# Performance work log

Measured on AMD Instinct MI355X. Metric: run time of the kernel, lower is better.

The kernel has to match this reference:

```python
import jax, jax.numpy as jnp
import numpy as np

B, C, H, W = 4, 32, 32, 1024
PATCH = 21           # patch_size in spatial_correlation_sample
DIL = 2              # dilation_patch
PAD = DIL * (PATCH - 1) // 2  # 20: max displacement, zero-padded out-of-range samples


def setup_inputs() -> dict:
    key = jax.random.key(0)
    k1, k2 = jax.random.split(key)
    x1 = jax.random.normal(k1, (B, C, H, W), dtype=jnp.float32)
    x2 = jax.random.normal(k2, (B, C, H, W), dtype=jnp.float32)
    return {"x1": x1, "x2": x2}


def _correlate(x1, x2):
    # spatial_correlation_sample(kernel_size=1, patch_size=21, stride=1,
    #                            padding=0, dilation_patch=2)
    # out[b, pi, pj, h, w] = sum_c x1[b,c,h,w] * x2[b,c,h+2*(pi-10), w+2*(pj-10)]
    # with out-of-bounds x2 samples treated as zero.
    b, c, h, w = x1.shape
    x2p = jnp.pad(x2, ((0, 0), (0, 0), (PAD, PAD), (PAD, PAD)))
    chans = []
    for i in range(PATCH):      # fixed 21x21 displacement grid (static slices)
        for j in range(PATCH):
            win = jax.lax.slice(x2p, (0, 0, DIL * i, DIL * j),
                                (b, c, DIL * i + h, DIL * j + w))
            chans.append(jnp.einsum('bchw,bchw->bhw', x1, win))
    corr = jnp.stack(chans, axis=1) / c  # (b, 441, h, w), normalized by n_channels
    return jax.nn.leaky_relu(corr, negative_slope=0.1)


def reference(x1, x2):
    # CorrelationNetwork.forward returns only out_correlation; the conv/deconv
    # flow pyramid does not contribute to the returned tensor (and the
    # visualize_flow calls reference undefined symbols in the original).
    return _correlate(x1, x2)
```

## Files before the change

### kernel.cpp

```cpp
#include <hip/hip_runtime.h>
#include <stdint.h>

#define BB     4
#define CC     32
#define HH     32
#define WW     1024
#define PATCH  21
#define DIL    2
#define RAD    10
#define PADW   20
#define CHUNKC 2
#define NP     (CC / CHUNKC)
#define NGR    266
#define ROWF   (NGR * 4)
#define BUFF   (CHUNKC * ROWF)

typedef __attribute__((address_space(3))) uint32_t lds_u32_t;
typedef __attribute__((address_space(1))) const uint32_t glb_u32_t;

__device__ __forceinline__ int swz(int s) { return s ^ ((s >> 3) & 1); }

__device__ __forceinline__ void stage_dma(const float* __restrict__ x2c0,
                                          float* __restrict__ sbuf, int tid) {
#pragma unroll
    for (int t = 0; t < 3; t++) {
        const int idx = tid + t * 256;
        if (idx < CHUNKC * NGR) {
            const int c  = (idx >= NGR) ? 1 : 0;
            const int q  = idx - c * NGR;
            const int gq = swz(q);
            const int base_gran = (tid & ~63) + t * 256;
            lds_u32_t* ldst = (lds_u32_t*)(sbuf + base_gran * 4);
            const float* src = x2c0 + (size_t)c * (HH * WW) + (gq * 4 - PADW);
            if (gq >= 5 && gq <= 260)
                __builtin_amdgcn_global_load_lds((glb_u32_t*)src, ldst, 16, 0, 0);
        }
    }
}

template <int PJ0, int NT, int NACC>
__device__ __forceinline__ void compute_half(const float* __restrict__ x1p,
                                             const float* __restrict__ sbuf,
                                             int tw, float (&acc)[NACC][8]) {
    constexpr int PJ0A = PJ0 & ~1;
    constexpr int DD   = 2 * (PJ0 - PJ0A);
    constexpr int NV4  = (DD + 8 + 2 * (NT - 1) + 3) / 4;
    const int g0 = 2 * tw + PJ0A / 2;
    int ps[NV4];
#pragma unroll
    for (int r = 0; r < NV4; r++) ps[r] = 4 * swz(g0 + r);

#pragma unroll
    for (int c = 0; c < CHUNKC; c++) {
        const float* xp = x1p + (size_t)c * (HH * WW);
        float4 a0 = *(const float4*)xp;
        float4 a1 = *(const float4*)(xp + 4);
        const float a[8] = {a0.x, a0.y, a0.z, a0.w, a1.x, a1.y, a1.z, a1.w};
        const float* row = sbuf + c * ROWF;
        float win[NV4 * 4];
#pragma unroll
        for (int r = 0; r < NV4; r++)
            *(float4*)&win[4 * r] = *(const float4*)(row + ps[r]);
#pragma unroll
        for (int j = 0; j < NT; j++)
#pragma unroll
            for (int k = 0; k < 8; k++)
                acc[j][k] = fmaf(a[k], win[DD + k + 2 * j], acc[j][k]);
    }
}

template <int NT, int NACC>
__device__ __forceinline__ void epilogue(float* __restrict__ outp,
                                         const float (&acc)[NACC][8], float inv_c) {
#pragma unroll
    for (int j = 0; j < NT; j++) {
        float4 o0, o1;
        float* p0 = (float*)&o0;
        float* p1 = (float*)&o1;
#pragma unroll
        for (int k = 0; k < 4; k++) {
            float v0 = acc[j][k] * inv_c;
            float v1 = acc[j][4 + k] * inv_c;
            p0[k] = v0 > 0.f ? v0 : 0.1f * v0;
            p1[k] = v1 > 0.f ? v1 : 0.1f * v1;
        }
        *(float4*)(outp + (size_t)j * HH * WW)     = o0;
        *(float4*)(outp + (size_t)j * HH * WW + 4) = o1;
    }
}

template <int PJ0_LO, int NT_LO, int PJ0_HI, int NT_HI>
__device__ __forceinline__ void corr_body(const float* __restrict__ x1,
                                          const float* __restrict__ x2,
                                          float* __restrict__ out,
                                          float* __restrict__ sx2) {
    const int tid = threadIdx.x;
    const int tw  = tid & 127;
    const int th2 = tid >> 7;
    const int h   = blockIdx.x;
    const int bp  = blockIdx.y;
    const int b   = bp / PATCH;
    const int pi  = bp - b * PATCH;
    const int r2  = h + DIL * (pi - RAD);
    const int w8  = tw * 8;
    const int PJ0 = th2 ? PJ0_HI : PJ0_LO;
    const int NT  = th2 ? NT_HI : NT_LO;

    float* outp = out + (((size_t)(b * PATCH * PATCH + pi * PATCH + PJ0)) * HH + h) * WW + w8;

    if ((unsigned)r2 >= (unsigned)HH) {
        float4 z = make_float4(0.f, 0.f, 0.f, 0.f);
        for (int j = 0; j < NT; j++) {
            *(float4*)(outp + (size_t)j * HH * WW)     = z;
            *(float4*)(outp + (size_t)j * HH * WW + 4) = z;
        }
        return;
    }

    if (tid < 40) {
        const int rr = tid / 10, g = tid % 10;
        const int slot = (g < 5) ? g : (256 + g);
        float4 z = make_float4(0.f, 0.f, 0.f, 0.f);
        *(float4*)(sx2 + rr * ROWF + 4 * slot) = z;
    }

    const float* x2base = x2 + ((size_t)(b * CC) * HH + r2) * WW;
    const float* x1base = x1 + ((size_t)(b * CC) * HH + h) * WW + w8;

    stage_dma(x2base, sx2, tid);
    __syncthreads();

    float acc[NT_LO][8];
#pragma unroll
    for (int j = 0; j < NT_LO; j++)
#pragma unroll
        for (int k = 0; k < 8; k++) acc[j][k] = 0.f;

    for (int p = 0; p < NP; p++) {
        if (p + 1 < NP)
            stage_dma(x2base + (size_t)(p + 1) * CHUNKC * HH * WW,
                      sx2 + ((p + 1) & 1) * BUFF, tid);
        const float* bufc = sx2 + (p & 1) * BUFF;
        const float* x1p  = x1base + (size_t)p * CHUNKC * HH * WW;
        if (th2 == 0) compute_half<PJ0_LO, NT_LO>(x1p, bufc, tw, acc);
        else          compute_half<PJ0_HI, NT_HI>(x1p, bufc, tw, acc);
        if (p + 1 < NP) __syncthreads();
    }

    const float inv_c = 1.0f / (float)CC;
    if (th2 == 0) epilogue<NT_LO>(outp, acc, inv_c);
    else          epilogue<NT_HI>(outp, acc, inv_c);
}

__global__ __launch_bounds__(256, 6)
void corr_kernel(const float* __restrict__ x1, const float* __restrict__ x2,
                 float* __restrict__ out) {
    __shared__ float sx2[2 * BUFF];
    if (blockIdx.z == 0)      corr_body<0, 4, 4, 4>(x1, x2, out, sx2);
    else if (blockIdx.z == 1) corr_body<8, 4, 12, 4>(x1, x2, out, sx2);
    else                      corr_body<16, 3, 19, 2>(x1, x2, out, sx2);
}

extern "C" void kernel_launch(void* const* d_in, const int* in_sizes, int n_in,
                              void* d_out, int out_size, void* d_ws, size_t ws_size,
                              hipStream_t stream) {
    const float* x1 = (const float*)d_in[0];
    const float* x2 = (const float*)d_in[1];
    float* out = (float*)d_out;

    dim3 grid(HH, BB * PATCH, 3);
    dim3 block(256, 1, 1);
    corr_kernel<<<grid, block, 0, stream>>>(x1, x2, out);
}
```

Baseline: 341.5 us.

## Merge pj split into one 512-thread block covering all 21 offsets

Replaces the three-way blockIdx.z split of pj offsets with a single 512-thread block. Four thread groups cover pj ranges 0-5, 6-10, 11-15 and 16-20, so each staged x2 row is loaded once per (b,h,pi) instead of three times. Channel chunks double to 4 per pipeline stage and the LDS swizzle gains extra bits to spread bank conflicts. This cuts redundant x2 staging and x1 reloads at the cost of more registers per thread (6x8 accumulators), fewer resident waves, and a grid remap that orders blocks by h and pi.

```diff
diff --git a/kernel.cpp b/kernel.cpp
--- a/kernel.cpp
+++ b/kernel.cpp
@@ -9,7 +9,7 @@
 #define DIL    2
 #define RAD    10
 #define PADW   20
-#define CHUNKC 2
+#define CHUNKC 4
 #define NP     (CC / CHUNKC)
 #define NGR    266
 #define ROWF   (NGR * 4)
@@ -18,18 +18,20 @@
 typedef __attribute__((address_space(3))) uint32_t lds_u32_t;
 typedef __attribute__((address_space(1))) const uint32_t glb_u32_t;
 
-__device__ __forceinline__ int swz(int s) { return s ^ ((s >> 3) & 1); }
+__device__ __forceinline__ int swz(int s) {
+    return s ^ ((s >> 3) & 1) ^ (((s >> 4) & 3) << 1);
+}
 
 __device__ __forceinline__ void stage_dma(const float* __restrict__ x2c0,
                                           float* __restrict__ sbuf, int tid) {
 #pragma unroll
     for (int t = 0; t < 3; t++) {
-        const int idx = tid + t * 256;
+        const int idx = tid + t * 512;
         if (idx < CHUNKC * NGR) {
-            const int c  = (idx >= NGR) ? 1 : 0;
+            const int c  = idx / NGR;
             const int q  = idx - c * NGR;
             const int gq = swz(q);
-            const int base_gran = (tid & ~63) + t * 256;
+            const int base_gran = (tid & ~63) + t * 512;
             lds_u32_t* ldst = (lds_u32_t*)(sbuf + base_gran * 4);
             const float* src = x2c0 + (size_t)c * (HH * WW) + (gq * 4 - PADW);
             if (gq >= 5 && gq <= 260)
@@ -38,25 +40,22 @@
     }
 }
 
-template <int PJ0, int NT, int NACC>
-__device__ __forceinline__ void compute_half(const float* __restrict__ x1p,
-                                             const float* __restrict__ sbuf,
-                                             int tw, float (&acc)[NACC][8]) {
+template <int PJ0, int NT>
+__device__ __forceinline__ void compute_pass(const float* __restrict__ x1p,
+                                             const float* __restrict__ bufc,
+                                             const int (&ps)[5],
+                                             float (&acc)[6][8]) {
     constexpr int PJ0A = PJ0 & ~1;
     constexpr int DD   = 2 * (PJ0 - PJ0A);
     constexpr int NV4  = (DD + 8 + 2 * (NT - 1) + 3) / 4;
-    const int g0 = 2 * tw + PJ0A / 2;
-    int ps[NV4];
-#pragma unroll
-    for (int r = 0; r < NV4; r++) ps[r] = 4 * swz(g0 + r);
-
+    static_assert(NV4 <= 5, "ps[] too small");
 #pragma unroll
     for (int c = 0; c < CHUNKC; c++) {
         const float* xp = x1p + (size_t)c * (HH * WW);
         float4 a0 = *(const float4*)xp;
         float4 a1 = *(const float4*)(xp + 4);
         const float a[8] = {a0.x, a0.y, a0.z, a0.w, a1.x, a1.y, a1.z, a1.w};
-        const float* row = sbuf + c * ROWF;
+        const float* row = bufc + c * ROWF;
         float win[NV4 * 4];
 #pragma unroll
         for (int r = 0; r < NV4; r++)
@@ -69,9 +68,9 @@
     }
 }
 
-template <int NT, int NACC>
+template <int NT>
 __device__ __forceinline__ void epilogue(float* __restrict__ outp,
-                                         const float (&acc)[NACC][8], float inv_c) {
+                                         const float (&acc)[6][8], float inv_c) {
 #pragma unroll
     for (int j = 0; j < NT; j++) {
         float4 o0, o1;
@@ -89,40 +88,49 @@
     }
 }
 
-template <int PJ0_LO, int NT_LO, int PJ0_HI, int NT_HI>
-__device__ __forceinline__ void corr_body(const float* __restrict__ x1,
-                                          const float* __restrict__ x2,
-                                          float* __restrict__ out,
-                                          float* __restrict__ sx2) {
+__global__ __launch_bounds__(512, 4)
+void corr_kernel(const float* __restrict__ x1, const float* __restrict__ x2,
+                 float* __restrict__ out) {
+    __shared__ float sx2[2 * BUFF];
+
     const int tid = threadIdx.x;
     const int tw  = tid & 127;
-    const int th2 = tid >> 7;
-    const int h   = blockIdx.x;
-    const int bp  = blockIdx.y;
-    const int b   = bp / PATCH;
-    const int pi  = bp - b * PATCH;
+    const int th4 = tid >> 7;
+
+    const int b   = blockIdx.x >> 1;
+    const int hh  = blockIdx.x & 1;
+    const int by  = blockIdx.y;
+    const int pi  = by % PATCH;
+    const int h   = hh * 16 + by / PATCH;
     const int r2  = h + DIL * (pi - RAD);
     const int w8  = tw * 8;
-    const int PJ0 = th2 ? PJ0_HI : PJ0_LO;
-    const int NT  = th2 ? NT_HI : NT_LO;
 
-    float* outp = out + (((size_t)(b * PATCH * PATCH + pi * PATCH + PJ0)) * HH + h) * WW + w8;
+    const int PJ0r = (th4 == 0) ? 0 : (th4 == 1) ? 6 : (th4 == 2) ? 11 : 16;
+    const int NTr  = (th4 == 0) ? 6 : 5;
+
+    float* outp = out + (((size_t)(b * PATCH * PATCH + pi * PATCH + PJ0r)) * HH + h) * WW + w8;
 
     if ((unsigned)r2 >= (unsigned)HH) {
         float4 z = make_float4(0.f, 0.f, 0.f, 0.f);
-        for (int j = 0; j < NT; j++) {
+        for (int j = 0; j < NTr; j++) {
             *(float4*)(outp + (size_t)j * HH * WW)     = z;
             *(float4*)(outp + (size_t)j * HH * WW + 4) = z;
         }
         return;
     }
 
-    if (tid < 40) {
+    if (tid < 80) {
         const int rr = tid / 10, g = tid % 10;
         const int slot = (g < 5) ? g : (256 + g);
         float4 z = make_float4(0.f, 0.f, 0.f, 0.f);
         *(float4*)(sx2 + rr * ROWF + 4 * slot) = z;
     }
+
+    const int pj0a2 = (th4 == 0) ? 0 : (th4 == 1) ? 3 : (th4 == 2) ? 5 : 8;
+    const int g0 = 2 * tw + pj0a2;
+    int ps[5];
+#pragma unroll
+    for (int r = 0; r < 5; r++) ps[r] = 4 * swz(g0 + r);
 
     const float* x2base = x2 + ((size_t)(b * CC) * HH + r2) * WW;
     const float* x1base = x1 + ((size_t)(b * CC) * HH + h) * WW + w8;
@@ -130,9 +138,9 @@
     stage_dma(x2base, sx2, tid);
     __syncthreads();
 
-    float acc[NT_LO][8];
+    float acc[6][8];
 #pragma unroll
-    for (int j = 0; j < NT_LO; j++)
+    for (int j = 0; j < 6; j++)
 #pragma unroll
         for (int k = 0; k < 8; k++) acc[j][k] = 0.f;
 
@@ -142,23 +150,18 @@
                       sx2 + ((p + 1) & 1) * BUFF, tid);
         const float* bufc = sx2 + (p & 1) * BUFF;
         const float* x1p  = x1base + (size_t)p * CHUNKC * HH * WW;
-        if (th2 == 0) compute_half<PJ0_LO, NT_LO>(x1p, bufc, tw, acc);
-        else          compute_half<PJ0_HI, NT_HI>(x1p, bufc, tw, acc);
+        if (th4 == 0)      compute_pass<0,  6>(x1p, bufc, ps, acc);
+        else if (th4 == 1) compute_pass<6,  5>(x1p, bufc, ps, acc);
+        else if (th4 == 2) compute_pass<11, 5>(x1p, bufc, ps, acc);
+        else               compute_pass<16, 5>(x1p, bufc, ps, acc);
         if (p + 1 < NP) __syncthreads();
     }
 
     const float inv_c = 1.0f / (float)CC;
-    if (th2 == 0) epilogue<NT_LO>(outp, acc, inv_c);
-    else          epilogue<NT_HI>(outp, acc, inv_c);
-}
-
-__global__ __launch_bounds__(256, 6)
-void corr_kernel(const float* __restrict__ x1, const float* __restrict__ x2,
-                 float* __restrict__ out) {
-    __shared__ float sx2[2 * BUFF];
-    if (blockIdx.z == 0)      corr_body<0, 4, 4, 4>(x1, x2, out, sx2);
-    else if (blockIdx.z == 1) corr_body<8, 4, 12, 4>(x1, x2, out, sx2);
-    else                      corr_body<16, 3, 19, 2>(x1, x2, out, sx2);
+    if (th4 == 0)      epilogue<6>(outp, acc, inv_c);
+    else if (th4 == 1) epilogue<5>(outp, acc, inv_c);
+    else if (th4 == 2) epilogue<5>(outp, acc, inv_c);
+    else               epilogue<5>(outp, acc, inv_c);
 }
 
 extern "C" void kernel_launch(void* const* d_in, const int* in_sizes, int n_in,
@@ -168,7 +171,7 @@
     const float* x2 = (const float*)d_in[1];
     float* out = (float*)d_out;
 
-    dim3 grid(HH, BB * PATCH, 3);
-    dim3 block(256, 1, 1);
+    dim3 grid(8, (PATCH * 16), 1);
+    dim3 block(512, 1, 1);
     corr_kernel<<<grid, block, 0, stream>>>(x1, x2, out);
 }
```

After: 650.5 us. 90.5% more time.

## Index blocks by x2 row and share staged row across two output rows

Applied to the files above, without the earlier changes.

Blocks are now indexed by the x2 source row r2 instead of the output row h. Each staged x2 row in LDS then serves two (pi, h) output pairs that read the same row, halving the x2 staging per output. Each thread computes a 2x2 tile of pj displacements for two rows, and the grid becomes 72x32x6, with many blocks exiting early or idling on out-of-range slots. This cuts LDS and DMA traffic per output, at the cost of more accumulators, lower occupancy (launch bounds drop from 6 to 5) and wasted blocks.

```diff
diff --git a/kernel.cpp b/kernel.cpp
--- a/kernel.cpp
+++ b/kernel.cpp
@@ -6,7 +6,6 @@
 #define HH     32
 #define WW     1024
 #define PATCH  21
-#define DIL    2
 #define RAD    10
 #define PADW   20
 #define CHUNKC 2
@@ -14,13 +13,14 @@
 #define NGR    266
 #define ROWF   (NGR * 4)
 #define BUFF   (CHUNKC * ROWF)
+#define CSTR   (HH * WW)
 
 typedef __attribute__((address_space(3))) uint32_t lds_u32_t;
 typedef __attribute__((address_space(1))) const uint32_t glb_u32_t;
 
 __device__ __forceinline__ int swz(int s) { return s ^ ((s >> 3) & 1); }
 
-__device__ __forceinline__ void stage_dma(const float* __restrict__ x2c0,
+__device__ __forceinline__ void stage_dma(const float* __restrict__ src0,
                                           float* __restrict__ sbuf, int tid) {
 #pragma unroll
     for (int t = 0; t < 3; t++) {
@@ -30,89 +30,62 @@
             const int q  = idx - c * NGR;
             const int gq = swz(q);
             const int base_gran = (tid & ~63) + t * 256;
-            lds_u32_t* ldst = (lds_u32_t*)(sbuf + base_gran * 4);
-            const float* src = x2c0 + (size_t)c * (HH * WW) + (gq * 4 - PADW);
+            lds_u32_t* dst = (lds_u32_t*)(sbuf + base_gran * 4);
+            const float* src = src0 + (size_t)c * CSTR + (gq * 4 - PADW);
             if (gq >= 5 && gq <= 260)
-                __builtin_amdgcn_global_load_lds((glb_u32_t*)src, ldst, 16, 0, 0);
+                __builtin_amdgcn_global_load_lds((glb_u32_t*)src, dst, 16, 0, 0);
         }
     }
 }
 
-template <int PJ0, int NT, int NACC>
-__device__ __forceinline__ void compute_half(const float* __restrict__ x1p,
-                                             const float* __restrict__ sbuf,
-                                             int tw, float (&acc)[NACC][8]) {
-    constexpr int PJ0A = PJ0 & ~1;
-    constexpr int DD   = 2 * (PJ0 - PJ0A);
-    constexpr int NV4  = (DD + 8 + 2 * (NT - 1) + 3) / 4;
-    const int g0 = 2 * tw + PJ0A / 2;
-    int ps[NV4];
-#pragma unroll
-    for (int r = 0; r < NV4; r++) ps[r] = 4 * swz(g0 + r);
+__global__ __launch_bounds__(256, 5)
+void corr_kernel(const float* __restrict__ x1, const float* __restrict__ x2,
+                 float* __restrict__ out) {
+    __shared__ float sx2[2 * BUFF + 16];
 
-#pragma unroll
-    for (int c = 0; c < CHUNKC; c++) {
-        const float* xp = x1p + (size_t)c * (HH * WW);
-        float4 a0 = *(const float4*)xp;
-        float4 a1 = *(const float4*)(xp + 4);
-        const float a[8] = {a0.x, a0.y, a0.z, a0.w, a1.x, a1.y, a1.z, a1.w};
-        const float* row = sbuf + c * ROWF;
-        float win[NV4 * 4];
-#pragma unroll
-        for (int r = 0; r < NV4; r++)
-            *(float4*)&win[4 * r] = *(const float4*)(row + ps[r]);
-#pragma unroll
-        for (int j = 0; j < NT; j++)
-#pragma unroll
-            for (int k = 0; k < 8; k++)
-                acc[j][k] = fmaf(a[k], win[DD + k + 2 * j], acc[j][k]);
-    }
-}
-
-template <int NT, int NACC>
-__device__ __forceinline__ void epilogue(float* __restrict__ outp,
-                                         const float (&acc)[NACC][8], float inv_c) {
-#pragma unroll
-    for (int j = 0; j < NT; j++) {
-        float4 o0, o1;
-        float* p0 = (float*)&o0;
-        float* p1 = (float*)&o1;
-#pragma unroll
-        for (int k = 0; k < 4; k++) {
-            float v0 = acc[j][k] * inv_c;
-            float v1 = acc[j][4 + k] * inv_c;
-            p0[k] = v0 > 0.f ? v0 : 0.1f * v0;
-            p1[k] = v1 > 0.f ? v1 : 0.1f * v1;
-        }
-        *(float4*)(outp + (size_t)j * HH * WW)     = o0;
-        *(float4*)(outp + (size_t)j * HH * WW + 4) = o1;
-    }
-}
-
-template <int PJ0_LO, int NT_LO, int PJ0_HI, int NT_HI>
-__device__ __forceinline__ void corr_body(const float* __restrict__ x1,
-                                          const float* __restrict__ x2,
-                                          float* __restrict__ out,
-                                          float* __restrict__ sx2) {
     const int tid = threadIdx.x;
     const int tw  = tid & 127;
     const int th2 = tid >> 7;
-    const int h   = blockIdx.x;
-    const int bp  = blockIdx.y;
-    const int b   = bp / PATCH;
-    const int pi  = bp - b * PATCH;
-    const int r2  = h + DIL * (pi - RAD);
-    const int w8  = tw * 8;
-    const int PJ0 = th2 ? PJ0_HI : PJ0_LO;
-    const int NT  = th2 ? NT_HI : NT_LO;
+    const int r2  = (int)blockIdx.x - PADW;
+    const int b   = blockIdx.y >> 3;
+    const int s   = blockIdx.y & 7;
+    const int z   = blockIdx.z;
 
-    float* outp = out + (((size_t)(b * PATCH * PATCH + pi * PATCH + PJ0)) * HH + h) * WW + w8;
+    const int pi_hi = min(20, (r2 + 20) >> 1);
+    const int pi_lo = max(0, (r2 - 10) >> 1);
+    const int L     = pi_hi - pi_lo + 1;
+    const int e0    = 2 * s;
+    if (e0 >= L) return;
+
+    const int  pi0  = pi_hi - e0;
+    const int  h0   = r2 + 20 - 2 * pi0;
+    const bool has1 = (e0 + 1) < L;
+    const int  pi1  = pi0 - 1;
+    const int  h1   = h0 + 2;
+
+    const int  pjb    = 4 * z + 2 * th2;
+    const bool st0    = (pjb     <= 20);
+    const bool st1    = (pjb + 1 <= 20);
+    const bool active = st0;
+    const int  w8     = tw * 8;
+
+    float* out0 = out + (((size_t)(b * PATCH * PATCH + pi0 * PATCH + pjb)) * HH + h0) * WW + w8;
+    float* out1 = out + (((size_t)(b * PATCH * PATCH + pi1 * PATCH + pjb)) * HH + h1) * WW + w8;
 
     if ((unsigned)r2 >= (unsigned)HH) {
-        float4 z = make_float4(0.f, 0.f, 0.f, 0.f);
-        for (int j = 0; j < NT; j++) {
-            *(float4*)(outp + (size_t)j * HH * WW)     = z;
-            *(float4*)(outp + (size_t)j * HH * WW + 4) = z;
+        float4 zv = make_float4(0.f, 0.f, 0.f, 0.f);
+        if (active) {
+#pragma unroll
+            for (int j = 0; j < 2; j++) {
+                if (j == 0 ? st0 : st1) {
+                    *(float4*)(out0 + (size_t)j * CSTR)     = zv;
+                    *(float4*)(out0 + (size_t)j * CSTR + 4) = zv;
+                    if (has1) {
+                        *(float4*)(out1 + (size_t)j * CSTR)     = zv;
+                        *(float4*)(out1 + (size_t)j * CSTR + 4) = zv;
+                    }
+                }
+            }
         }
         return;
     }
@@ -120,45 +93,87 @@
     if (tid < 40) {
         const int rr = tid / 10, g = tid % 10;
         const int slot = (g < 5) ? g : (256 + g);
-        float4 z = make_float4(0.f, 0.f, 0.f, 0.f);
-        *(float4*)(sx2 + rr * ROWF + 4 * slot) = z;
+        *(float4*)(sx2 + rr * ROWF + 4 * slot) = make_float4(0.f, 0.f, 0.f, 0.f);
     }
 
+    const int g0 = active ? (2 * tw + 2 * z + th2) : (2 * tw);
+    int ps0 = 4 * swz(g0), ps1 = 4 * swz(g0 + 1), ps2 = 4 * swz(g0 + 2);
+
     const float* x2base = x2 + ((size_t)(b * CC) * HH + r2) * WW;
-    const float* x1base = x1 + ((size_t)(b * CC) * HH + h) * WW + w8;
+    const float* x1p0   = x1 + ((size_t)(b * CC) * HH + h0) * WW + w8;
+    const float* x1p1   = has1 ? (x1p0 + 2 * WW) : x1p0;
 
     stage_dma(x2base, sx2, tid);
     __syncthreads();
 
-    float acc[NT_LO][8];
+    float acc0[2][8], acc1[2][8];
 #pragma unroll
-    for (int j = 0; j < NT_LO; j++)
+    for (int j = 0; j < 2; j++)
 #pragma unroll
-        for (int k = 0; k < 8; k++) acc[j][k] = 0.f;
+        for (int k = 0; k < 8; k++) { acc0[j][k] = 0.f; acc1[j][k] = 0.f; }
 
     for (int p = 0; p < NP; p++) {
         if (p + 1 < NP)
-            stage_dma(x2base + (size_t)(p + 1) * CHUNKC * HH * WW,
+            stage_dma(x2base + (size_t)(p + 1) * CHUNKC * CSTR,
                       sx2 + ((p + 1) & 1) * BUFF, tid);
-        const float* bufc = sx2 + (p & 1) * BUFF;
-        const float* x1p  = x1base + (size_t)p * CHUNKC * HH * WW;
-        if (th2 == 0) compute_half<PJ0_LO, NT_LO>(x1p, bufc, tw, acc);
-        else          compute_half<PJ0_HI, NT_HI>(x1p, bufc, tw, acc);
+        if (active) {
+            const float* buf = sx2 + (p & 1) * BUFF;
+#pragma unroll
+            for (int c = 0; c < CHUNKC; c++) {
+                const float* row = buf + c * ROWF;
+                float win[12];
+                *(float4*)&win[0] = *(const float4*)(row + ps0);
+                *(float4*)&win[4] = *(const float4*)(row + ps1);
+                *(float4*)&win[8] = *(const float4*)(row + ps2);
+
+                const float* xa = x1p0 + (size_t)(CHUNKC * p + c) * CSTR;
+                const float* xb = x1p1 + (size_t)(CHUNKC * p + c) * CSTR;
+                float4 a00 = *(const float4*)xa, a01 = *(const float4*)(xa + 4);
+                float4 a10 = *(const float4*)xb, a11 = *(const float4*)(xb + 4);
+                const float a0[8] = {a00.x, a00.y, a00.z, a00.w, a01.x, a01.y, a01.z, a01.w};
+                const float a1[8] = {a10.x, a10.y, a10.z, a10.w, a11.x, a11.y, a11.z, a11.w};
+
+#pragma unroll
+                for (int j = 0; j < 2; j++)
+#pragma unroll
+                    for (int k = 0; k < 8; k++) {
+                        const float wv = win[k + 2 * j];
+                        acc0[j][k] = fmaf(a0[k], wv, acc0[j][k]);
+                        acc1[j][k] = fmaf(a1[k], wv, acc1[j][k]);
+                    }
+            }
+        }
         if (p + 1 < NP) __syncthreads();
     }
 
+    if (!active) return;
+
     const float inv_c = 1.0f / (float)CC;
-    if (th2 == 0) epilogue<NT_LO>(outp, acc, inv_c);
-    else          epilogue<NT_HI>(outp, acc, inv_c);
-}
-
-__global__ __launch_bounds__(256, 6)
-void corr_kernel(const float* __restrict__ x1, const float* __restrict__ x2,
-                 float* __restrict__ out) {
-    __shared__ float sx2[2 * BUFF];
-    if (blockIdx.z == 0)      corr_body<0, 4, 4, 4>(x1, x2, out, sx2);
-    else if (blockIdx.z == 1) corr_body<8, 4, 12, 4>(x1, x2, out, sx2);
-    else                      corr_body<16, 3, 19, 2>(x1, x2, out, sx2);
+#pragma unroll
+    for (int j = 0; j < 2; j++) {
+        if (j == 0 ? st0 : st1) {
+            float4 o0, o1, q0, q1;
+            float* po0 = (float*)&o0; float* po1 = (float*)&o1;
+            float* pq0 = (float*)&q0; float* pq1 = (float*)&q1;
+#pragma unroll
+            for (int k = 0; k < 4; k++) {
+                float v0 = acc0[j][k]     * inv_c;
+                float v1 = acc0[j][4 + k] * inv_c;
+                float u0 = acc1[j][k]     * inv_c;
+                float u1 = acc1[j][4 + k] * inv_c;
+                po0[k] = v0 > 0.f ? v0 : 0.1f * v0;
+                po1[k] = v1 > 0.f ? v1 : 0.1f * v1;
+                pq0[k] = u0 > 0.f ? u0 : 0.1f * u0;
+                pq1[k] = u1 > 0.f ? u1 : 0.1f * u1;
+            }
+            *(float4*)(out0 + (size_t)j * CSTR)     = o0;
+            *(float4*)(out0 + (size_t)j * CSTR + 4) = o1;
+            if (has1) {
+                *(float4*)(out1 + (size_t)j * CSTR)     = q0;
+                *(float4*)(out1 + (size_t)j * CSTR + 4) = q1;
+            }
+        }
+    }
 }
 
 extern "C" void kernel_launch(void* const* d_in, const int* in_sizes, int n_in,
@@ -168,7 +183,7 @@
     const float* x2 = (const float*)d_in[1];
     float* out = (float*)d_out;
 
-    dim3 grid(HH, BB * PATCH, 3);
+    dim3 grid(72, BB * 8, 6);
     dim3 block(256, 1, 1);
     corr_kernel<<<grid, block, 0, stream>>>(x1, x2, out);
 }
```

Result: slower. 385.4 us (+12.9%).
